# Optimization experiments

Measured on AMD Instinct MI355X. Metric: run time of the kernel, lower is better.

## Reference

```python
import jax, jax.numpy as jnp
import numpy as np
import math

D_MODEL = 128
N_HEAD = 8
D_K = D_MODEL // N_HEAD
NEG_INF = -1e30


def setup_inputs() -> dict:
    key = jax.random.key(0)
    ks = jax.random.split(key, 8)
    B, N, D = 4, 2048, D_MODEL
    s = 1.0 / math.sqrt(D)
    x = jax.random.normal(ks[0], (B, D, N), dtype=jnp.float32)
    mask = jnp.ones((B, N), dtype=jnp.float32)
    Wq = jax.random.normal(ks[1], (D, D), dtype=jnp.float32) * s
    Wk = jax.random.normal(ks[2], (D, D), dtype=jnp.float32) * s
    Wv = jax.random.normal(ks[3], (D, D), dtype=jnp.float32) * s
    Wfc = jax.random.normal(ks[4], (D, D), dtype=jnp.float32) * s
    z = jnp.zeros((D,), dtype=jnp.float32)
    return {"x": x, "mask": mask, "Wq": Wq, "bq": z, "Wk": Wk, "bk": z,
            "Wv": Wv, "bv": z, "Wfc": Wfc, "bfc": z}


def reference(x, mask, Wq, bq, Wk, bk, Wv, bv, Wfc, bfc):
    # x: [B, D, N], mask: [B, N]
    B, D, N = x.shape
    xt = jnp.swapaxes(x, 1, 2)  # [B, N, D]
    q = (xt @ Wq.T + bq).reshape(B, N, N_HEAD, D_K)
    k = (xt @ Wk.T + bk).reshape(B, N, N_HEAD, D_K)
    v = (xt @ Wv.T + bv).reshape(B, N, N_HEAD, D_K)
    # scores: [B, H, Nq, Nk]; NOTE: original scales by sqrt(d_model), not sqrt(d_k)
    scores = jnp.einsum('bnhd,bmhd->bhnm', q, k) / jnp.sqrt(jnp.float32(D))
    # multiplicative mask_logits over the key dimension
    m = mask[:, None, None, :]  # [B, 1, 1, Nk]
    scores = scores * m + (1.0 - m) * NEG_INF
    atten = jax.nn.softmax(scores, axis=-1)  # dropout is identity (p=0 / eval)
    out = jnp.einsum('bhnm,bmhd->bnhd', atten, v).reshape(B, N, D)
    out = out @ Wfc.T + bfc
    return jnp.swapaxes(out, 1, 2)  # [B, D, N]
```

## Files before the change

### kernel.cpp

```cpp
#include <hip/hip_runtime.h>
#include <stdint.h>

#define BSZ  4
#define NSEQ 2048
#define DM   128
#define NH   8
#define DK   16
#define LOG2E 1.4426950408889634f
#define SCALE_QL 0.1275156338341935f
#define W_SCALE 3.814697265625e-6f

typedef __bf16          bf16x8v __attribute__((ext_vector_type(8)));
typedef float           f32x4   __attribute__((ext_vector_type(4)));
typedef float           f32x16  __attribute__((ext_vector_type(16)));
typedef unsigned short  u16x8   __attribute__((ext_vector_type(8)));
typedef unsigned short  u16x4   __attribute__((ext_vector_type(4)));
typedef unsigned int    u32x2   __attribute__((ext_vector_type(2)));
typedef unsigned int    u32x4   __attribute__((ext_vector_type(4)));

__device__ __forceinline__ unsigned short f2bf(float f) {
    unsigned u = __float_as_uint(f);
    u = (u + 0x7fffu + ((u >> 16) & 1u)) >> 16;
    return (unsigned short)u;
}

__device__ __forceinline__ unsigned int pack2bf(float a, float b) {
#if __has_builtin(__builtin_amdgcn_cvt_pk_bf16_f32)
    typedef __bf16 bf16x2 __attribute__((ext_vector_type(2)));
    bf16x2 v = __builtin_amdgcn_cvt_pk_bf16_f32(a, b);
    return __builtin_bit_cast(unsigned int, v);
#else
    return (unsigned)f2bf(a) | ((unsigned)f2bf(b) << 16);
#endif
}

__device__ __forceinline__ float exp2_(float x) {
#if __has_builtin(__builtin_amdgcn_exp2f)
    return __builtin_amdgcn_exp2f(x);
#else
    return exp2f(x);
#endif
}

__device__ __forceinline__ u16x8 cvt8(const float* p, float sc) {
    const f32x4 a = *reinterpret_cast<const f32x4*>(p);
    const f32x4 b = *reinterpret_cast<const f32x4*>(p + 4);
    u32x4 u = {pack2bf(a[0] * sc, a[1] * sc), pack2bf(a[2] * sc, a[3] * sc),
               pack2bf(b[0] * sc, b[1] * sc), pack2bf(b[2] * sc, b[3] * sc)};
    return __builtin_bit_cast(u16x8, u);
}

__device__ __forceinline__ f32x4 mfma16(u16x8 a, u16x8 b, f32x4 c) {
    return __builtin_amdgcn_mfma_f32_16x16x32_bf16(
        __builtin_bit_cast(bf16x8v, a), __builtin_bit_cast(bf16x8v, b), c, 0, 0, 0);
}
__device__ __forceinline__ f32x16 mfma32(u16x8 a, u16x8 b, f32x16 c) {
    return __builtin_amdgcn_mfma_f32_32x32x16_bf16(
        __builtin_bit_cast(bf16x8v, a), __builtin_bit_cast(bf16x8v, b), c, 0, 0, 0);
}

__global__ __launch_bounds__(768) void k_qkv(
    const float* __restrict__ x,
    const float* __restrict__ Wq, const float* __restrict__ bq,
    const float* __restrict__ Wk, const float* __restrict__ bk,
    const float* __restrict__ Wv, const float* __restrict__ bv,
    const float* __restrict__ Wfc, const float* __restrict__ mask,
    unsigned short* __restrict__ Q, unsigned short* __restrict__ Kb,
    unsigned short* __restrict__ Vt,
    unsigned short* __restrict__ WfcB, unsigned short* __restrict__ wb)
{
    __shared__ __align__(16) float xs[DM * 36];
    const int tid = threadIdx.x;

    const int gt = blockIdx.x * 768 + tid;
    if (gt < DM * DM) {
        WfcB[gt] = f2bf(Wfc[gt]);
    } else if (gt < DM * DM + BSZ * NSEQ) {
        const int i = gt - DM * DM;
        wb[i] = f2bf(mask[i] * W_SCALE);
    }

    const int b  = blockIdx.x >> 6;
    const int n0 = (blockIdx.x & 63) << 5;

#pragma unroll
    for (int i = tid; i < 1024; i += 768) {
        const int d = i >> 3, c4 = (i & 7) << 2;
        *reinterpret_cast<f32x4*>(&xs[d * 36 + c4]) =
            *reinterpret_cast<const f32x4*>(x + (size_t)(b * DM + d) * NSEQ + n0 + c4);
    }
    __syncthreads();

    const int lane = tid & 63;
    const int wv   = tid >> 6;
    const int mat  = wv >> 2;
    const int nt   = (wv >> 1) & 1;
    const int th   = wv & 1;
    const int c    = lane & 15;
    const int quad = lane >> 4;
    const int col  = n0 + nt * 16 + c;

    u16x8 xf[4];
#pragma unroll
    for (int kk = 0; kk < 4; ++kk) {
        float f[8];
#pragma unroll
        for (int j = 0; j < 8; ++j)
            f[j] = xs[(kk * 32 + quad * 8 + j) * 36 + nt * 16 + c];
        u32x4 u = {pack2bf(f[0], f[1]), pack2bf(f[2], f[3]),
                   pack2bf(f[4], f[5]), pack2bf(f[6], f[7])};
        xf[kk] = __builtin_bit_cast(u16x8, u);
    }

    const float* W    = (mat == 0) ? Wq : (mat == 1) ? Wk : Wv;
    const float* bias = (mat == 0) ? bq : (mat == 1) ? bk : bv;
    const float  sc   = (mat == 0) ? SCALE_QL : 1.0f;
    const float  vw   = (mat == 2) ? mask[b * NSEQ + col] * W_SCALE : 0.f;

#pragma unroll
    for (int tt = 0; tt < 4; ++tt) {
        const int t = th * 4 + tt;
        f32x4 acc = {0.f, 0.f, 0.f, 0.f};
#pragma unroll
        for (int kk = 0; kk < 4; ++kk)
            acc = mfma16(cvt8(W + (t * 16 + c) * DM + kk * 32 + quad * 8, sc),
                         xf[kk], acc);
        if (mat == 2) {
#pragma unroll
            for (int r = 0; r < 4; ++r)
                Vt[((b * NH + t) * DK + quad * 4 + r) * NSEQ + col] =
                    f2bf((acc[r] + bias[t * 16 + quad * 4 + r]) * vw);
        } else {
            u16x4 pk;
#pragma unroll
            for (int r = 0; r < 4; ++r)
                pk[r] = f2bf(acc[r] + bias[t * 16 + quad * 4 + r] * sc);
            *reinterpret_cast<u16x4*>(
                (mat == 0 ? Q : Kb) + ((size_t)(b * NH + t) * NSEQ + col) * DK +
                quad * 4) = pk;
        }
    }
}

__global__ __launch_bounds__(256, 4) void k_attn(
    const unsigned short* __restrict__ Q,
    const unsigned short* __restrict__ Kb,
    const unsigned short* __restrict__ Vt,
    const unsigned short* __restrict__ wb,
    unsigned short* __restrict__ AO)
{
    __shared__ __align__(16) char smem[17408];
    const int tid  = threadIdx.x;
    const int lane = tid & 63;
    const int w    = tid >> 6;
    const int q32  = lane & 31;
    const int c    = lane & 15;
    const int quad = lane >> 4;
    const int hi   = lane >> 5;

    const int b  = blockIdx.x >> 9;
    const int h  = (blockIdx.x >> 6) & 7;
    const int n0 = (blockIdx.x & 63) << 5;
    const int bh = b * NH + h;

    const u16x8 uq = *reinterpret_cast<const u16x8*>(
        Q + ((size_t)bh * NSEQ + n0 + q32) * DK + 8 * hi);

    const unsigned short* Kp = Kb + (size_t)bh * NSEQ * DK + 8 * hi;
    const unsigned short* Vp = Vt + ((size_t)bh * DK + c) * NSEQ + 8 * quad;
    const unsigned short* wp = wb + b * NSEQ + 8 * quad;

    char* pbase = smem + w * 4352;
    char* wrow  = pbase + q32 * 136 + 8 * hi;
    const char* rrow0 = pbase + c * 136 + 16 * quad;
    const char* rrow1 = pbase + (c + 16) * 136 + 16 * quad;

    f32x4 o0 = {0.f, 0.f, 0.f, 0.f}, o1 = {0.f, 0.f, 0.f, 0.f};
    f32x4 l0 = {0.f, 0.f, 0.f, 0.f}, l1 = {0.f, 0.f, 0.f, 0.f};
    const f32x16 z16 = {};
    const int kvb = w * (NSEQ / 4);

    u16x8 nk0 = *reinterpret_cast<const u16x8*>(Kp + (size_t)(kvb + q32) * DK);
    u16x8 nk1 = *reinterpret_cast<const u16x8*>(Kp + (size_t)(kvb + 32 + q32) * DK);

    for (int it = 0; it < 8; ++it) {
        const int kv0 = kvb + it * 64;
        const u16x8 uk0 = nk0, uk1 = nk1;
        if (it < 7) {
            nk0 = *reinterpret_cast<const u16x8*>(Kp + (size_t)(kv0 + 64 + q32) * DK);
            nk1 = *reinterpret_cast<const u16x8*>(Kp + (size_t)(kv0 + 96 + q32) * DK);
        }
        f32x16 S0 = mfma32(uk0, uq, z16);
        f32x16 S1 = mfma32(uk1, uq, z16);

#pragma unroll
        for (int i = 0; i < 16; ++i) {
            S0[i] = exp2_(S0[i]);
            S1[i] = exp2_(S1[i]);
        }

#pragma unroll
        for (int g = 0; g < 4; ++g) {
            u32x2 d0 = {pack2bf(S0[4 * g], S0[4 * g + 1]),
                        pack2bf(S0[4 * g + 2], S0[4 * g + 3])};
            u32x2 d1 = {pack2bf(S1[4 * g], S1[4 * g + 1]),
                        pack2bf(S1[4 * g + 2], S1[4 * g + 3])};
            *reinterpret_cast<u32x2*>(wrow + 16 * g) = d0;
            *reinterpret_cast<u32x2*>(wrow + 64 + 16 * g) = d1;
        }

#pragma unroll
        for (int t = 0; t < 2; ++t) {
            const u16x8 uv  = *reinterpret_cast<const u16x8*>(Vp + kv0 + 32 * t);
            const u16x8 uw  = *reinterpret_cast<const u16x8*>(wp + kv0 + 32 * t);
            const u16x8 up0 = *reinterpret_cast<const u16x8*>(rrow0 + 64 * t);
            const u16x8 up1 = *reinterpret_cast<const u16x8*>(rrow1 + 64 * t);
            o0 = mfma16(uv, up0, o0);
            o1 = mfma16(uv, up1, o1);
            l0 = mfma16(uw, up0, l0);
            l1 = mfma16(uw, up1, l1);
        }
    }

    __syncthreads();
    float* Lsm = reinterpret_cast<float*>(smem);
    float* Osm = reinterpret_cast<float*>(smem + 512);
    Lsm[w * 32 + c]      = l0[0];
    Lsm[w * 32 + 16 + c] = l1[0];
    *reinterpret_cast<f32x4*>(Osm + w * 640 + c * 20 + 4 * quad)        = o0;
    *reinterpret_cast<f32x4*>(Osm + w * 640 + (c + 16) * 20 + 4 * quad) = o1;
    __syncthreads();

    const int q   = tid >> 3;
    const int dk2 = (tid & 7) * 2;
    const float l = Lsm[q] + Lsm[32 + q] + Lsm[64 + q] + Lsm[96 + q];
    const float* Oq = Osm + q * 20 + dk2;
    const float v0 = Oq[0] + Oq[640] + Oq[1280] + Oq[1920];
    const float v1 = Oq[1] + Oq[641] + Oq[1281] + Oq[1921];
    const float inv = 1.0f / l;
    *reinterpret_cast<unsigned int*>(
        AO + ((size_t)(b * NSEQ) + n0 + q) * DM + h * DK + dk2) =
        pack2bf(v0 * inv, v1 * inv);
}

__global__ __launch_bounds__(256) void k_fc(
    const unsigned short* __restrict__ AO,
    const unsigned short* __restrict__ WfcB, const float* __restrict__ bfc,
    float* __restrict__ out)
{
    const int lane = threadIdx.x & 63;
    const int w    = threadIdx.x >> 6;
    const int c    = lane & 15;
    const int quad = lane >> 4;
    const int b    = blockIdx.x >> 8;
    const int n0   = ((blockIdx.x >> 1) & 127) << 4;
    const int t    = (blockIdx.x & 1) * 4 + w;

    u16x8 af[4];
#pragma unroll
    for (int kk = 0; kk < 4; ++kk)
        af[kk] = *reinterpret_cast<const u16x8*>(
            AO + ((size_t)(b * NSEQ) + n0 + c) * DM + kk * 32 + quad * 8);

    f32x4 acc = {0.f, 0.f, 0.f, 0.f};
#pragma unroll
    for (int kk = 0; kk < 4; ++kk)
        acc = mfma16(*reinterpret_cast<const u16x8*>(
                         WfcB + (t * 16 + c) * DM + kk * 32 + quad * 8),
                     af[kk], acc);
#pragma unroll
    for (int r = 0; r < 4; ++r)
        out[(size_t)(b * DM + t * 16 + quad * 4 + r) * NSEQ + n0 + c] =
            acc[r] + bfc[t * 16 + quad * 4 + r];
}

extern "C" void kernel_launch(void* const* d_in, const int* in_sizes, int n_in,
                              void* d_out, int out_size, void* d_ws, size_t ws_size,
                              hipStream_t stream)
{
    const float* x    = (const float*)d_in[0];
    const float* mask = (const float*)d_in[1];
    const float* Wq   = (const float*)d_in[2];
    const float* bq   = (const float*)d_in[3];
    const float* Wk   = (const float*)d_in[4];
    const float* bk   = (const float*)d_in[5];
    const float* Wv   = (const float*)d_in[6];
    const float* bv   = (const float*)d_in[7];
    const float* Wfc  = (const float*)d_in[8];
    const float* bfc  = (const float*)d_in[9];
    float* out = (float*)d_out;

    const size_t QKV_ELEMS = (size_t)BSZ * NH * NSEQ * DK;
    unsigned short* Q    = (unsigned short*)d_ws;
    unsigned short* Kb   = Q + QKV_ELEMS;
    unsigned short* Vt   = Kb + QKV_ELEMS;
    unsigned short* AO   = Vt + QKV_ELEMS;
    unsigned short* WfcB = AO + QKV_ELEMS;
    unsigned short* wb   = WfcB + DM * DM;

    k_qkv<<<256, 768, 0, stream>>>(x, Wq, bq, Wk, bk, Wv, bv, Wfc, mask,
                                   Q, Kb, Vt, WfcB, wb);
    k_attn<<<2048, 256, 0, stream>>>(Q, Kb, Vt, wb, AO);
    k_fc<<<1024, 256, 0, stream>>>(AO, WfcB, bfc, out);
}
```

Baseline: 131.7 us.

## Process two query tiles per attention block to reuse K/V loads

Each attention block now handles 64 queries (two 32-query tiles) instead of 32, so every K, V and mask fragment loaded from global memory feeds twice as many MFMAs. The grid is halved to 1024 blocks and shared memory per block doubles to hold both tiles' probability and reduction buffers. This cuts redundant K/V global traffic, but it raises register and LDS pressure, which may lower occupancy and gives fewer blocks to spread across the CUs.

After: 134.1 us. About the same (+1.8%).

```diff
diff --git a/kernel.cpp b/kernel.cpp
--- a/kernel.cpp
+++ b/kernel.cpp
@@ -149,7 +149,7 @@
     const unsigned short* __restrict__ wb,
     unsigned short* __restrict__ AO)
 {
-    __shared__ __align__(16) char smem[17408];
+    __shared__ __align__(16) char smem[34816];
     const int tid  = threadIdx.x;
     const int lane = tid & 63;
     const int w    = tid >> 6;
@@ -158,25 +158,34 @@
     const int quad = lane >> 4;
     const int hi   = lane >> 5;
 
-    const int b  = blockIdx.x >> 9;
-    const int h  = (blockIdx.x >> 6) & 7;
-    const int n0 = (blockIdx.x & 63) << 5;
-    const int bh = b * NH + h;
-
-    const u16x8 uq = *reinterpret_cast<const u16x8*>(
+    const int qt0 = blockIdx.x * 2;
+    const int b   = qt0 >> 9;
+    const int h   = (qt0 >> 6) & 7;
+    const int n0  = (qt0 & 63) << 5;
+    const int bh  = b * NH + h;
+
+    const u16x8 uqA = *reinterpret_cast<const u16x8*>(
         Q + ((size_t)bh * NSEQ + n0 + q32) * DK + 8 * hi);
+    const u16x8 uqB = *reinterpret_cast<const u16x8*>(
+        Q + ((size_t)bh * NSEQ + n0 + 32 + q32) * DK + 8 * hi);
 
     const unsigned short* Kp = Kb + (size_t)bh * NSEQ * DK + 8 * hi;
     const unsigned short* Vp = Vt + ((size_t)bh * DK + c) * NSEQ + 8 * quad;
     const unsigned short* wp = wb + b * NSEQ + 8 * quad;
 
-    char* pbase = smem + w * 4352;
-    char* wrow  = pbase + q32 * 136 + 8 * hi;
-    const char* rrow0 = pbase + c * 136 + 16 * quad;
-    const char* rrow1 = pbase + (c + 16) * 136 + 16 * quad;
-
-    f32x4 o0 = {0.f, 0.f, 0.f, 0.f}, o1 = {0.f, 0.f, 0.f, 0.f};
-    f32x4 l0 = {0.f, 0.f, 0.f, 0.f}, l1 = {0.f, 0.f, 0.f, 0.f};
+    char* pbA = smem + w * 8704;
+    char* pbB = pbA + 4352;
+    char* wrowA = pbA + q32 * 136 + 8 * hi;
+    char* wrowB = pbB + q32 * 136 + 8 * hi;
+    const char* rA0 = pbA + c * 136 + 16 * quad;
+    const char* rA1 = pbA + (c + 16) * 136 + 16 * quad;
+    const char* rB0 = pbB + c * 136 + 16 * quad;
+    const char* rB1 = pbB + (c + 16) * 136 + 16 * quad;
+
+    f32x4 oA0 = {0.f, 0.f, 0.f, 0.f}, oA1 = {0.f, 0.f, 0.f, 0.f};
+    f32x4 oB0 = {0.f, 0.f, 0.f, 0.f}, oB1 = {0.f, 0.f, 0.f, 0.f};
+    f32x4 lA0 = {0.f, 0.f, 0.f, 0.f}, lA1 = {0.f, 0.f, 0.f, 0.f};
+    f32x4 lB0 = {0.f, 0.f, 0.f, 0.f}, lB1 = {0.f, 0.f, 0.f, 0.f};
     const f32x16 z16 = {};
     const int kvb = w * (NSEQ / 4);
 
@@ -190,57 +199,93 @@
             nk0 = *reinterpret_cast<const u16x8*>(Kp + (size_t)(kv0 + 64 + q32) * DK);
             nk1 = *reinterpret_cast<const u16x8*>(Kp + (size_t)(kv0 + 96 + q32) * DK);
         }
-        f32x16 S0 = mfma32(uk0, uq, z16);
-        f32x16 S1 = mfma32(uk1, uq, z16);
-
-#pragma unroll
-        for (int i = 0; i < 16; ++i) {
-            S0[i] = exp2_(S0[i]);
-            S1[i] = exp2_(S1[i]);
-        }
-
-#pragma unroll
-        for (int g = 0; g < 4; ++g) {
-            u32x2 d0 = {pack2bf(S0[4 * g], S0[4 * g + 1]),
-                        pack2bf(S0[4 * g + 2], S0[4 * g + 3])};
-            u32x2 d1 = {pack2bf(S1[4 * g], S1[4 * g + 1]),
-                        pack2bf(S1[4 * g + 2], S1[4 * g + 3])};
-            *reinterpret_cast<u32x2*>(wrow + 16 * g) = d0;
-            *reinterpret_cast<u32x2*>(wrow + 64 + 16 * g) = d1;
+
+        {
+            f32x16 SA = mfma32(uk0, uqA, z16);
+            f32x16 SB = mfma32(uk0, uqB, z16);
+#pragma unroll
+            for (int j = 0; j < 16; ++j) {
+                SA[j] = exp2_(SA[j]);
+                SB[j] = exp2_(SB[j]);
+            }
+#pragma unroll
+            for (int g = 0; g < 4; ++g) {
+                u32x2 dA = {pack2bf(SA[4 * g], SA[4 * g + 1]),
+                            pack2bf(SA[4 * g + 2], SA[4 * g + 3])};
+                u32x2 dB = {pack2bf(SB[4 * g], SB[4 * g + 1]),
+                            pack2bf(SB[4 * g + 2], SB[4 * g + 3])};
+                *reinterpret_cast<u32x2*>(wrowA + 16 * g) = dA;
+                *reinterpret_cast<u32x2*>(wrowB + 16 * g) = dB;
+            }
+        }
+        {
+            f32x16 SA = mfma32(uk1, uqA, z16);
+            f32x16 SB = mfma32(uk1, uqB, z16);
+#pragma unroll
+            for (int j = 0; j < 16; ++j) {
+                SA[j] = exp2_(SA[j]);
+                SB[j] = exp2_(SB[j]);
+            }
+#pragma unroll
+            for (int g = 0; g < 4; ++g) {
+                u32x2 dA = {pack2bf(SA[4 * g], SA[4 * g + 1]),
+                            pack2bf(SA[4 * g + 2], SA[4 * g + 3])};
+                u32x2 dB = {pack2bf(SB[4 * g], SB[4 * g + 1]),
+                            pack2bf(SB[4 * g + 2], SB[4 * g + 3])};
+                *reinterpret_cast<u32x2*>(wrowA + 64 + 16 * g) = dA;
+                *reinterpret_cast<u32x2*>(wrowB + 64 + 16 * g) = dB;
+            }
         }
 
 #pragma unroll
         for (int t = 0; t < 2; ++t) {
-            const u16x8 uv  = *reinterpret_cast<const u16x8*>(Vp + kv0 + 32 * t);
-            const u16x8 uw  = *reinterpret_cast<const u16x8*>(wp + kv0 + 32 * t);
-            const u16x8 up0 = *reinterpret_cast<const u16x8*>(rrow0 + 64 * t);
-            const u16x8 up1 = *reinterpret_cast<const u16x8*>(rrow1 + 64 * t);
-            o0 = mfma16(uv, up0, o0);
-            o1 = mfma16(uv, up1, o1);
-            l0 = mfma16(uw, up0, l0);
-            l1 = mfma16(uw, up1, l1);
+            const u16x8 uv = *reinterpret_cast<const u16x8*>(Vp + kv0 + 32 * t);
+            const u16x8 uw = *reinterpret_cast<const u16x8*>(wp + kv0 + 32 * t);
+            const u16x8 upA0 = *reinterpret_cast<const u16x8*>(rA0 + 64 * t);
+            const u16x8 upA1 = *reinterpret_cast<const u16x8*>(rA1 + 64 * t);
+            const u16x8 upB0 = *reinterpret_cast<const u16x8*>(rB0 + 64 * t);
+            const u16x8 upB1 = *reinterpret_cast<const u16x8*>(rB1 + 64 * t);
+            oA0 = mfma16(uv, upA0, oA0);
+            oB0 = mfma16(uv, upB0, oB0);
+            oA1 = mfma16(uv, upA1, oA1);
+            oB1 = mfma16(uv, upB1, oB1);
+            lA0 = mfma16(uw, upA0, lA0);
+            lB0 = mfma16(uw, upB0, lB0);
+            lA1 = mfma16(uw, upA1, lA1);
+            lB1 = mfma16(uw, upB1, lB1);
         }
     }
 
     __syncthreads();
-    float* Lsm = reinterpret_cast<float*>(smem);
-    float* Osm = reinterpret_cast<float*>(smem + 512);
-    Lsm[w * 32 + c]      = l0[0];
-    Lsm[w * 32 + 16 + c] = l1[0];
-    *reinterpret_cast<f32x4*>(Osm + w * 640 + c * 20 + 4 * quad)        = o0;
-    *reinterpret_cast<f32x4*>(Osm + w * 640 + (c + 16) * 20 + 4 * quad) = o1;
+    float* LsmA = reinterpret_cast<float*>(smem);
+    float* LsmB = reinterpret_cast<float*>(smem + 512);
+    float* OsmA = reinterpret_cast<float*>(smem + 1024);
+    float* OsmB = reinterpret_cast<float*>(smem + 1024 + 10240);
+    LsmA[w * 32 + c]      = lA0[0];
+    LsmA[w * 32 + 16 + c] = lA1[0];
+    LsmB[w * 32 + c]      = lB0[0];
+    LsmB[w * 32 + 16 + c] = lB1[0];
+    *reinterpret_cast<f32x4*>(OsmA + w * 640 + c * 20 + 4 * quad)        = oA0;
+    *reinterpret_cast<f32x4*>(OsmA + w * 640 + (c + 16) * 20 + 4 * quad) = oA1;
+    *reinterpret_cast<f32x4*>(OsmB + w * 640 + c * 20 + 4 * quad)        = oB0;
+    *reinterpret_cast<f32x4*>(OsmB + w * 640 + (c + 16) * 20 + 4 * quad) = oB1;
     __syncthreads();
 
     const int q   = tid >> 3;
     const int dk2 = (tid & 7) * 2;
-    const float l = Lsm[q] + Lsm[32 + q] + Lsm[64 + q] + Lsm[96 + q];
-    const float* Oq = Osm + q * 20 + dk2;
-    const float v0 = Oq[0] + Oq[640] + Oq[1280] + Oq[1920];
-    const float v1 = Oq[1] + Oq[641] + Oq[1281] + Oq[1921];
-    const float inv = 1.0f / l;
-    *reinterpret_cast<unsigned int*>(
-        AO + ((size_t)(b * NSEQ) + n0 + q) * DM + h * DK + dk2) =
-        pack2bf(v0 * inv, v1 * inv);
+#pragma unroll
+    for (int i = 0; i < 2; ++i) {
+        const float* Lsm = i ? LsmB : LsmA;
+        const float* Osm = i ? OsmB : OsmA;
+        const float l = Lsm[q] + Lsm[32 + q] + Lsm[64 + q] + Lsm[96 + q];
+        const float* Oq = Osm + q * 20 + dk2;
+        const float v0 = Oq[0] + Oq[640] + Oq[1280] + Oq[1920];
+        const float v1 = Oq[1] + Oq[641] + Oq[1281] + Oq[1921];
+        const float inv = 1.0f / l;
+        *reinterpret_cast<unsigned int*>(
+            AO + ((size_t)(b * NSEQ) + n0 + i * 32 + q) * DM + h * DK + dk2) =
+            pack2bf(v0 * inv, v1 * inv);
+    }
 }
 
 __global__ __launch_bounds__(256) void k_fc(
@@ -300,6 +345,6 @@
 
     k_qkv<<<256, 768, 0, stream>>>(x, Wq, bq, Wk, bk, Wv, bv, Wfc, mask,
                                    Q, Kb, Vt, WfcB, wb);
-    k_attn<<<2048, 256, 0, stream>>>(Q, Kb, Vt, wb, AO);
+    k_attn<<<1024, 256, 0, stream>>>(Q, Kb, Vt, wb, AO);
     k_fc<<<1024, 256, 0, stream>>>(AO, WfcB, bfc, out);
 }
```

## Fuse output projection into attention kernel via last-block atomic counter

Applied to the files above, without the earlier changes.

Removes the separate k_fc launch. Each attention block increments a per-(batch, 32-row tile) counter, and the eighth block to finish, after all heads for those rows are written, computes the Wfc projection for the 32 rows. This is meant to cut one kernel launch and its tail. In exchange it adds a memset launch, atomics and fences, and a serial FC tail on the last-arriving blocks.

Result: slower. 215.1 us (+63.3%).

```diff
diff --git a/kernel.cpp b/kernel.cpp
--- a/kernel.cpp
+++ b/kernel.cpp
@@ -147,9 +147,14 @@
     const unsigned short* __restrict__ Kb,
     const unsigned short* __restrict__ Vt,
     const unsigned short* __restrict__ wb,
-    unsigned short* __restrict__ AO)
+    const unsigned short* __restrict__ WfcB,
+    const float* __restrict__ bfc,
+    unsigned short* __restrict__ AO,
+    float* __restrict__ out,
+    unsigned* __restrict__ cnt)
 {
     __shared__ __align__(16) char smem[17408];
+    __shared__ int fcflag;
     const int tid  = threadIdx.x;
     const int lane = tid & 63;
     const int w    = tid >> 6;
@@ -241,37 +246,42 @@
     *reinterpret_cast<unsigned int*>(
         AO + ((size_t)(b * NSEQ) + n0 + q) * DM + h * DK + dk2) =
         pack2bf(v0 * inv, v1 * inv);
-}
-
-__global__ __launch_bounds__(256) void k_fc(
-    const unsigned short* __restrict__ AO,
-    const unsigned short* __restrict__ WfcB, const float* __restrict__ bfc,
-    float* __restrict__ out)
-{
-    const int lane = threadIdx.x & 63;
-    const int w    = threadIdx.x >> 6;
-    const int c    = lane & 15;
-    const int quad = lane >> 4;
-    const int b    = blockIdx.x >> 8;
-    const int n0   = ((blockIdx.x >> 1) & 127) << 4;
-    const int t    = (blockIdx.x & 1) * 4 + w;
-
-    u16x8 af[4];
-#pragma unroll
-    for (int kk = 0; kk < 4; ++kk)
-        af[kk] = *reinterpret_cast<const u16x8*>(
-            AO + ((size_t)(b * NSEQ) + n0 + c) * DM + kk * 32 + quad * 8);
-
-    f32x4 acc = {0.f, 0.f, 0.f, 0.f};
-#pragma unroll
-    for (int kk = 0; kk < 4; ++kk)
-        acc = mfma16(*reinterpret_cast<const u16x8*>(
-                         WfcB + (t * 16 + c) * DM + kk * 32 + quad * 8),
-                     af[kk], acc);
-#pragma unroll
-    for (int r = 0; r < 4; ++r)
-        out[(size_t)(b * DM + t * 16 + quad * 4 + r) * NSEQ + n0 + c] =
-            acc[r] + bfc[t * 16 + quad * 4 + r];
+
+    __syncthreads();
+    if (tid == 0) {
+        __threadfence();
+        const unsigned old = __hip_atomic_fetch_add(
+            &cnt[b * 64 + (blockIdx.x & 63)], 1u,
+            __ATOMIC_RELAXED, __HIP_MEMORY_SCOPE_AGENT);
+        fcflag = (old == NH - 1);
+    }
+    __syncthreads();
+    if (!fcflag) return;
+
+    __threadfence();
+#pragma unroll
+    for (int ns = 0; ns < 2; ++ns) {
+        const int nc = n0 + ns * 16 + c;
+        u16x8 af[4];
+#pragma unroll
+        for (int kk = 0; kk < 4; ++kk)
+            af[kk] = *reinterpret_cast<const u16x8*>(
+                AO + ((size_t)(b * NSEQ) + nc) * DM + kk * 32 + quad * 8);
+#pragma unroll
+        for (int tt = 0; tt < 2; ++tt) {
+            const int t = w * 2 + tt;
+            f32x4 acc = {0.f, 0.f, 0.f, 0.f};
+#pragma unroll
+            for (int kk = 0; kk < 4; ++kk)
+                acc = mfma16(*reinterpret_cast<const u16x8*>(
+                                 WfcB + (t * 16 + c) * DM + kk * 32 + quad * 8),
+                             af[kk], acc);
+#pragma unroll
+            for (int r = 0; r < 4; ++r)
+                out[(size_t)(b * DM + t * 16 + quad * 4 + r) * NSEQ + nc] =
+                    acc[r] + bfc[t * 16 + quad * 4 + r];
+        }
+    }
 }
 
 extern "C" void kernel_launch(void* const* d_in, const int* in_sizes, int n_in,
@@ -297,9 +307,10 @@
     unsigned short* AO   = Vt + QKV_ELEMS;
     unsigned short* WfcB = AO + QKV_ELEMS;
     unsigned short* wb   = WfcB + DM * DM;
-
+    unsigned*       cnt  = (unsigned*)(wb + BSZ * NSEQ);
+
+    hipMemsetAsync(cnt, 0, 256 * sizeof(unsigned), stream);
     k_qkv<<<256, 768, 0, stream>>>(x, Wq, bq, Wk, bk, Wv, bv, Wfc, mask,
                                    Q, Kb, Vt, WfcB, wb);
-    k_attn<<<2048, 256, 0, stream>>>(Q, Kb, Vt, wb, AO);
-    k_fc<<<1024, 256, 0, stream>>>(AO, WfcB, bfc, out);
-}
+    k_attn<<<2048, 256, 0, stream>>>(Q, Kb, Vt, wb, WfcB, bfc, AO, out, cnt);
+}
```

## Keep softmax probabilities in registers and fold mask row-sum into PV MFMA

Applied to the files above, without the earlier changes.

Attention now keeps the exponentiated scores in registers instead of staging them through LDS. A cross-half-wave shuffle rearranges the packed bf16 values into the B operand of a 32x32x16 MFMA. V is stored as a 32-row-per-head buffer whose row 16 holds the mask weight, so the denominator comes out of the same MFMA as the output instead of separate l0/l1 MFMAs. This removes the LDS write/read of P and the separate mask-weight buffer. In exchange, roughly half of each MFMA's rows (17..31) compute unused garbage, and the V workspace doubles in size.

After: 132.4 us. Within noise of the previous version (+0.5%).

```diff
diff --git a/kernel.cpp b/kernel.cpp
--- a/kernel.cpp
+++ b/kernel.cpp
@@ -15,7 +15,6 @@
 typedef float           f32x16  __attribute__((ext_vector_type(16)));
 typedef unsigned short  u16x8   __attribute__((ext_vector_type(8)));
 typedef unsigned short  u16x4   __attribute__((ext_vector_type(4)));
-typedef unsigned int    u32x2   __attribute__((ext_vector_type(2)));
 typedef unsigned int    u32x4   __attribute__((ext_vector_type(4)));
 
 __device__ __forceinline__ unsigned short f2bf(float f) {
@@ -66,19 +65,14 @@
     const float* __restrict__ Wv, const float* __restrict__ bv,
     const float* __restrict__ Wfc, const float* __restrict__ mask,
     unsigned short* __restrict__ Q, unsigned short* __restrict__ Kb,
-    unsigned short* __restrict__ Vt,
-    unsigned short* __restrict__ WfcB, unsigned short* __restrict__ wb)
+    unsigned short* __restrict__ VW,
+    unsigned short* __restrict__ WfcB)
 {
     __shared__ __align__(16) float xs[DM * 36];
     const int tid = threadIdx.x;
 
     const int gt = blockIdx.x * 768 + tid;
-    if (gt < DM * DM) {
-        WfcB[gt] = f2bf(Wfc[gt]);
-    } else if (gt < DM * DM + BSZ * NSEQ) {
-        const int i = gt - DM * DM;
-        wb[i] = f2bf(mask[i] * W_SCALE);
-    }
+    if (gt < DM * DM) WfcB[gt] = f2bf(Wfc[gt]);
 
     const int b  = blockIdx.x >> 6;
     const int n0 = (blockIdx.x & 63) << 5;
@@ -128,8 +122,10 @@
         if (mat == 2) {
 #pragma unroll
             for (int r = 0; r < 4; ++r)
-                Vt[((b * NH + t) * DK + quad * 4 + r) * NSEQ + col] =
+                VW[((size_t)(b * NH + t) * 32 + quad * 4 + r) * NSEQ + col] =
                     f2bf((acc[r] + bias[t * 16 + quad * 4 + r]) * vw);
+            if (quad == 0)
+                VW[((size_t)(b * NH + t) * 32 + 16) * NSEQ + col] = f2bf(vw);
         } else {
             u16x4 pk;
 #pragma unroll
@@ -145,17 +141,15 @@
 __global__ __launch_bounds__(256, 4) void k_attn(
     const unsigned short* __restrict__ Q,
     const unsigned short* __restrict__ Kb,
-    const unsigned short* __restrict__ Vt,
-    const unsigned short* __restrict__ wb,
+    const unsigned short* __restrict__ VW,
     unsigned short* __restrict__ AO)
 {
-    __shared__ __align__(16) char smem[17408];
+    __shared__ float Lsm[128];
+    __shared__ __align__(16) float Osm[4 * 640];
     const int tid  = threadIdx.x;
     const int lane = tid & 63;
     const int w    = tid >> 6;
     const int q32  = lane & 31;
-    const int c    = lane & 15;
-    const int quad = lane >> 4;
     const int hi   = lane >> 5;
 
     const int b  = blockIdx.x >> 9;
@@ -167,16 +161,10 @@
         Q + ((size_t)bh * NSEQ + n0 + q32) * DK + 8 * hi);
 
     const unsigned short* Kp = Kb + (size_t)bh * NSEQ * DK + 8 * hi;
-    const unsigned short* Vp = Vt + ((size_t)bh * DK + c) * NSEQ + 8 * quad;
-    const unsigned short* wp = wb + b * NSEQ + 8 * quad;
-
-    char* pbase = smem + w * 4352;
-    char* wrow  = pbase + q32 * 136 + 8 * hi;
-    const char* rrow0 = pbase + c * 136 + 16 * quad;
-    const char* rrow1 = pbase + (c + 16) * 136 + 16 * quad;
-
-    f32x4 o0 = {0.f, 0.f, 0.f, 0.f}, o1 = {0.f, 0.f, 0.f, 0.f};
-    f32x4 l0 = {0.f, 0.f, 0.f, 0.f}, l1 = {0.f, 0.f, 0.f, 0.f};
+    const unsigned short* Ap =
+        VW + ((size_t)bh * 32 + q32) * NSEQ + 8 * hi;
+
+    f32x16 D = {};
     const f32x16 z16 = {};
     const int kvb = w * (NSEQ / 4);
 
@@ -190,45 +178,42 @@
             nk0 = *reinterpret_cast<const u16x8*>(Kp + (size_t)(kv0 + 64 + q32) * DK);
             nk1 = *reinterpret_cast<const u16x8*>(Kp + (size_t)(kv0 + 96 + q32) * DK);
         }
+        u16x8 av[4];
+#pragma unroll
+        for (int cc = 0; cc < 4; ++cc)
+            av[cc] = *reinterpret_cast<const u16x8*>(Ap + kv0 + 16 * cc);
+
         f32x16 S0 = mfma32(uk0, uq, z16);
         f32x16 S1 = mfma32(uk1, uq, z16);
 
-#pragma unroll
-        for (int i = 0; i < 16; ++i) {
-            S0[i] = exp2_(S0[i]);
-            S1[i] = exp2_(S1[i]);
-        }
-
-#pragma unroll
-        for (int g = 0; g < 4; ++g) {
-            u32x2 d0 = {pack2bf(S0[4 * g], S0[4 * g + 1]),
-                        pack2bf(S0[4 * g + 2], S0[4 * g + 3])};
-            u32x2 d1 = {pack2bf(S1[4 * g], S1[4 * g + 1]),
-                        pack2bf(S1[4 * g + 2], S1[4 * g + 3])};
-            *reinterpret_cast<u32x2*>(wrow + 16 * g) = d0;
-            *reinterpret_cast<u32x2*>(wrow + 64 + 16 * g) = d1;
-        }
-
-#pragma unroll
-        for (int t = 0; t < 2; ++t) {
-            const u16x8 uv  = *reinterpret_cast<const u16x8*>(Vp + kv0 + 32 * t);
-            const u16x8 uw  = *reinterpret_cast<const u16x8*>(wp + kv0 + 32 * t);
-            const u16x8 up0 = *reinterpret_cast<const u16x8*>(rrow0 + 64 * t);
-            const u16x8 up1 = *reinterpret_cast<const u16x8*>(rrow1 + 64 * t);
-            o0 = mfma16(uv, up0, o0);
-            o1 = mfma16(uv, up1, o1);
-            l0 = mfma16(uw, up0, l0);
-            l1 = mfma16(uw, up1, l1);
-        }
-    }
-
-    __syncthreads();
-    float* Lsm = reinterpret_cast<float*>(smem);
-    float* Osm = reinterpret_cast<float*>(smem + 512);
-    Lsm[w * 32 + c]      = l0[0];
-    Lsm[w * 32 + 16 + c] = l1[0];
-    *reinterpret_cast<f32x4*>(Osm + w * 640 + c * 20 + 4 * quad)        = o0;
-    *reinterpret_cast<f32x4*>(Osm + w * 640 + (c + 16) * 20 + 4 * quad) = o1;
+        unsigned int pk[16];
+#pragma unroll
+        for (int i = 0; i < 8; ++i) {
+            const float a0 = exp2_(S0[2 * i]),     a1 = exp2_(S0[2 * i + 1]);
+            const float b0 = exp2_(S1[2 * i]),     b1 = exp2_(S1[2 * i + 1]);
+            pk[i]     = pack2bf(a0, a1);
+            pk[8 + i] = pack2bf(b0, b1);
+        }
+
+#pragma unroll
+        for (int cc = 0; cc < 4; ++cc) {
+            const unsigned int q0 = pk[4 * cc + 0], q1 = pk[4 * cc + 1];
+            const unsigned int q2 = pk[4 * cc + 2], q3 = pk[4 * cc + 3];
+            const unsigned int t0 = (unsigned)__shfl_xor((int)q0, 32, 64);
+            const unsigned int t1 = (unsigned)__shfl_xor((int)q1, 32, 64);
+            const unsigned int t2 = (unsigned)__shfl_xor((int)q2, 32, 64);
+            const unsigned int t3 = (unsigned)__shfl_xor((int)q3, 32, 64);
+            u32x4 bf = {hi ? t2 : q0, hi ? t3 : q1,
+                        hi ? q2 : t0, hi ? q3 : t1};
+            D = mfma32(av[cc], __builtin_bit_cast(u16x8, bf), D);
+        }
+    }
+
+    if (!hi) Lsm[w * 32 + q32] = D[8];
+    *reinterpret_cast<f32x4*>(&Osm[w * 640 + q32 * 20 + 4 * hi]) =
+        f32x4{D[0], D[1], D[2], D[3]};
+    *reinterpret_cast<f32x4*>(&Osm[w * 640 + q32 * 20 + 8 + 4 * hi]) =
+        f32x4{D[4], D[5], D[6], D[7]};
     __syncthreads();
 
     const int q   = tid >> 3;
@@ -293,13 +278,12 @@
     const size_t QKV_ELEMS = (size_t)BSZ * NH * NSEQ * DK;
     unsigned short* Q    = (unsigned short*)d_ws;
     unsigned short* Kb   = Q + QKV_ELEMS;
-    unsigned short* Vt   = Kb + QKV_ELEMS;
-    unsigned short* AO   = Vt + QKV_ELEMS;
+    unsigned short* VW   = Kb + QKV_ELEMS;
+    unsigned short* AO   = VW + 2 * QKV_ELEMS;
     unsigned short* WfcB = AO + QKV_ELEMS;
-    unsigned short* wb   = WfcB + DM * DM;
 
     k_qkv<<<256, 768, 0, stream>>>(x, Wq, bq, Wk, bk, Wv, bv, Wfc, mask,
-                                   Q, Kb, Vt, WfcB, wb);
-    k_attn<<<2048, 256, 0, stream>>>(Q, Kb, Vt, wb, AO);
+                                   Q, Kb, VW, WfcB);
+    k_attn<<<2048, 256, 0, stream>>>(Q, Kb, VW, AO);
     k_fc<<<1024, 256, 0, stream>>>(AO, WfcB, bfc, out);
 }
```
